# Optimization experiments

Measured on AMD Instinct MI355X. Metric: run time of the kernel, lower is better.

Reference implementation:

```python
import jax, jax.numpy as jnp
import numpy as np

NUM_GROUPS = 32
NUM_HEAD_CH = 64
EPS = 1e-5


def setup_inputs() -> dict:
    key = jax.random.key(0)
    k1, k2, k3 = jax.random.split(key, 3)
    B, C, H, W = 16, 512, 32, 32
    return {
        "x": jax.random.normal(k1, (B, C, H, W), dtype=jnp.float32),
        "norm_w": jnp.ones((C,), dtype=jnp.float32),
        "norm_b": jnp.zeros((C,), dtype=jnp.float32),
        "qkv_w": jax.random.normal(k2, (3 * C, C), dtype=jnp.float32) * 0.02,
        "qkv_b": jnp.zeros((3 * C,), dtype=jnp.float32),
        "proj_w": jax.random.normal(k3, (C, C), dtype=jnp.float32) * 0.02,
        "proj_b": jnp.zeros((C,), dtype=jnp.float32),
    }


def _group_norm(x, w, b):
    # x: [B, C, T]
    B, C, T = x.shape
    g = x.reshape(B, NUM_GROUPS, C // NUM_GROUPS, T)
    mean = g.mean(axis=(2, 3), keepdims=True)
    var = g.var(axis=(2, 3), keepdims=True)
    g = (g - mean) * jax.lax.rsqrt(var + EPS)
    return g.reshape(B, C, T) * w[None, :, None] + b[None, :, None]


def reference(x, norm_w, norm_b, qkv_w, qkv_b, proj_w, proj_b):
    B, C, Hs, Ws = x.shape
    T = Hs * Ws
    xr = x.reshape(B, C, T)
    xn = _group_norm(xr, norm_w, norm_b)
    # 1x1 conv == matmul over channel dim
    qkv = jnp.einsum('oc,bct->bot', qkv_w, xn) + qkv_b[None, :, None]  # [B, 3C, T]
    q, k, v = jnp.split(qkv, 3, axis=1)
    nH = C // NUM_HEAD_CH
    ch = NUM_HEAD_CH
    q = q.reshape(B * nH, ch, T)
    k = k.reshape(B * nH, ch, T)
    v = v.reshape(B * nH, ch, T)
    scale = 1.0 / np.sqrt(np.sqrt(ch)).astype(np.float32)
    # [BH, T, S] score matrix, softmax in float32 (matches torch .float())
    weight = jnp.einsum('bct,bcs->bts', q * scale, k * scale)
    weight = jax.nn.softmax(weight.astype(jnp.float32), axis=-1).astype(weight.dtype)
    a = jnp.einsum('bts,bcs->bct', weight, v).reshape(B, C, T)
    h = jnp.einsum('oc,bct->bot', proj_w, a) + proj_b[None, :, None]
    return (xr + h).reshape(B, C, Hs, Ws)
```

## Files before the change

kernel.cpp:

```cpp
#include <hip/hip_runtime.h>
#include <hip/hip_bf16.h>


typedef __bf16 bf16x8 __attribute__((ext_vector_type(8)));
typedef __bf16 bf16x4 __attribute__((ext_vector_type(4)));
typedef float f32x4 __attribute__((ext_vector_type(4)));

#define MFMA16(a, b, c) __builtin_amdgcn_mfma_f32_16x16x32_bf16((a), (b), (c), 0, 0, 0)

typedef const __attribute__((address_space(1))) unsigned int* gptr_t;
typedef __attribute__((address_space(3))) unsigned int* lptr_t;

__device__ __forceinline__ void gload16(const void* g, void* l) {
  __builtin_amdgcn_global_load_lds((gptr_t)g, (lptr_t)l, 16, 0, 0);
}

__global__ __launch_bounds__(256) void cvt_bf16_2(const float* __restrict__ s0,
                                                  __hip_bfloat16* __restrict__ d0,
                                                  int n0,
                                                  const float* __restrict__ s1,
                                                  __hip_bfloat16* __restrict__ d1,
                                                  int n1) {
  int i = blockIdx.x * 256 + threadIdx.x;
  const float* src;
  __hip_bfloat16* dst;
  if (i < n0) {
    src = s0; dst = d0;
  } else {
    i -= n0;
    if (i >= n1) return;
    src = s1; dst = d1;
  }
  float4 v = ((const float4*)src)[i];
  union { __hip_bfloat16 h[4]; uint2 u; } pk;
  pk.h[0] = __float2bfloat16(v.x);
  pk.h[1] = __float2bfloat16(v.y);
  pk.h[2] = __float2bfloat16(v.z);
  pk.h[3] = __float2bfloat16(v.w);
  *(uint2*)(dst + (size_t)i * 4) = pk.u;
}

__global__ __launch_bounds__(256) void gn_kernel(const float* __restrict__ x,
                                                 const float* __restrict__ nw,
                                                 const float* __restrict__ nb,
                                                 __hip_bfloat16* __restrict__ xnt) {
  const int blk = blockIdx.x;
  const int bb = blk >> 5, g = blk & 31;
  const int tid = threadIdx.x;
  const float4* xg = (const float4*)(x + ((size_t)bb * 512 + g * 16) * 1024);

  float4 vals[16];
  float s = 0.f, ss = 0.f;
#pragma unroll
  for (int k = 0; k < 16; ++k) {
    float4 v = xg[tid + 256 * k];
    vals[k] = v;
    s += v.x + v.y + v.z + v.w;
    ss += v.x * v.x + v.y * v.y + v.z * v.z + v.w * v.w;
  }
#pragma unroll
  for (int off = 1; off < 64; off <<= 1) {
    s += __shfl_xor(s, off, 64);
    ss += __shfl_xor(ss, off, 64);
  }
  __shared__ float red[8];
  const int wid = tid >> 6, lane = tid & 63;
  if (lane == 0) { red[wid] = s; red[wid + 4] = ss; }
  __syncthreads();
  s = red[0] + red[1] + red[2] + red[3];
  ss = red[4] + red[5] + red[6] + red[7];
  const float mean = s * (1.f / 16384.f);
  const float var = ss * (1.f / 16384.f) - mean * mean;
  const float rstd = rsqrtf(var + 1e-5f);

  float aa[16], cc[16];
#pragma unroll
  for (int k = 0; k < 16; ++k) {
    float w = nw[g * 16 + k];
    float b = nb[g * 16 + k];
    aa[k] = rstd * w;
    cc[k] = b - mean * aa[k];
  }
#pragma unroll
  for (int j = 0; j < 4; ++j) {
    union { __hip_bfloat16 h[16]; uint4 u[2]; } row;
#pragma unroll
    for (int k = 0; k < 16; ++k) {
      float v = ((const float*)&vals[k])[j];
      row.h[k] = __float2bfloat16(v * aa[k] + cc[k]);
    }
    size_t idx = ((size_t)bb * 1024 + 4 * tid + j) * 512 + g * 16;
    *(uint4*)(xnt + idx) = row.u[0];
    *(uint4*)(xnt + idx + 8) = row.u[1];
  }
}

template <int EPI>
__global__ __launch_bounds__(512) void gemm_bt(const __hip_bfloat16* __restrict__ A,
                                               const __hip_bfloat16* __restrict__ Bt,
                                               const float* __restrict__ bias,
                                               __hip_bfloat16* __restrict__ oq,
                                               __hip_bfloat16* __restrict__ ok,
                                               __hip_bfloat16* __restrict__ ov,
                                               const float* __restrict__ xres,
                                               float* __restrict__ of) {
  __shared__ __hip_bfloat16 Alds[128 * 64];
  __shared__ __hip_bfloat16 Blds[256 * 64];
  const int tid = threadIdx.x;
  const int wid = tid >> 6, lane = tid & 63;
  const int g = lane >> 4, tl = lane & 15;
  const int wr = wid >> 2, wc = wid & 3;
  const int NM = (EPI == 0) ? 12 : 4;
  const int id = blockIdx.x;
  const int xcd = id & 7, w = id >> 3;
  const int m0 = (w % NM) * 128;
  const int n0 = (xcd * 8 + w / NM) * 256;

  const int srow8 = lane >> 3;
  const int sselem = ((lane & 7) * 8) ^ (srow8 << 3);
  const int rswz = (tl & 7) << 4;

  f32x4 acc[4][4];
#pragma unroll
  for (int i = 0; i < 4; ++i)
#pragma unroll
    for (int j = 0; j < 4; ++j) acc[i][j] = (f32x4){0.f, 0.f, 0.f, 0.f};

  for (int kt = 0; kt < 8; ++kt) {
    const int k0 = kt * 64;
    __syncthreads();
#pragma unroll
    for (int q = 0; q < 2; ++q) {
      const int r = q * 64 + wid * 8 + srow8;
      gload16(A + (size_t)(m0 + r) * 512 + k0 + sselem,
              (char*)Alds + q * 8192 + wid * 1024);
    }
#pragma unroll
    for (int q = 0; q < 4; ++q) {
      const int r = q * 64 + wid * 8 + srow8;
      gload16(Bt + (size_t)(n0 + r) * 512 + k0 + sselem,
              (char*)Blds + q * 8192 + wid * 1024);
    }
    __syncthreads();
#pragma unroll
    for (int kk = 0; kk < 2; ++kk) {
      bf16x8 af[4], bfr[4];
#pragma unroll
      for (int mi = 0; mi < 4; ++mi) {
        const int row = wr * 64 + mi * 16 + tl;
        af[mi] = *(const bf16x8*)((char*)Alds + row * 128 + ((kk * 64 + g * 16) ^ rswz));
      }
#pragma unroll
      for (int ni = 0; ni < 4; ++ni) {
        const int row = wc * 64 + ni * 16 + tl;
        bfr[ni] = *(const bf16x8*)((char*)Blds + row * 128 + ((kk * 64 + g * 16) ^ rswz));
      }
      __builtin_amdgcn_s_setprio(1);
#pragma unroll
      for (int mi = 0; mi < 4; ++mi)
#pragma unroll
        for (int ni = 0; ni < 4; ++ni)
          acc[mi][ni] = MFMA16(af[mi], bfr[ni], acc[mi][ni]);
      __builtin_amdgcn_s_setprio(0);
    }
  }

  if (EPI == 0) {
    const bool isv = (m0 >= 1024);
    const bool isq = (m0 < 512);
    const float qs = 0.42466090014286f;
#pragma unroll
    for (int mi = 0; mi < 4; ++mi) {
      const int o = m0 + wr * 64 + mi * 16 + g * 4;
      const int och = o & 511, h = och >> 6, cb = och & 63;
#pragma unroll
      for (int ni = 0; ni < 4; ++ni) {
        const int n = n0 + wc * 64 + ni * 16 + tl;
        const int bb2 = n >> 10, t = n & 1023;
        const int bh = bb2 * 8 + h;
        if (!isv) {
          union { __hip_bfloat16 h4[4]; uint2 u; } pk;
#pragma unroll
          for (int r = 0; r < 4; ++r)
            pk.h4[r] = __float2bfloat16((acc[mi][ni][r] + bias[o + r]) * qs);
          __hip_bfloat16* dst = (isq ? oq : ok) + ((size_t)bh * 1024 + t) * 64 + cb;
          *(uint2*)dst = pk.u;
        } else {
#pragma unroll
          for (int r = 0; r < 4; ++r)
            ov[((size_t)bh * 64 + cb + r) * 1024 + t] =
                __float2bfloat16(acc[mi][ni][r] + bias[o + r]);
        }
      }
    }
  } else {
#pragma unroll
    for (int mi = 0; mi < 4; ++mi) {
#pragma unroll
      for (int r = 0; r < 4; ++r) {
        const int o = m0 + wr * 64 + mi * 16 + g * 4 + r;
        const float bv = bias[o];
#pragma unroll
        for (int ni = 0; ni < 4; ++ni) {
          const int n = n0 + wc * 64 + ni * 16 + tl;
          const int bb2 = n >> 10, t = n & 1023;
          const size_t xi = ((size_t)bb2 * 512 + o) * 1024 + t;
          of[xi] = xres[xi] + acc[mi][ni][r] + bv;
        }
      }
    }
  }
}

__global__ __launch_bounds__(512) void attn_kernel(const __hip_bfloat16* __restrict__ qt,
                                                   const __hip_bfloat16* __restrict__ kt,
                                                   const __hip_bfloat16* __restrict__ vv,
                                                   __hip_bfloat16* __restrict__ at) {
  const int blk = blockIdx.x;
  const int xcd = blk & 7;
  const int within = blk >> 3;
  const int tile = within & 3;
  const int bhi = xcd * 16 + (within >> 2);
  const int tid = threadIdx.x;
  const int wid = tid >> 6, lane = tid & 63;
  const int g = lane >> 4, tl = lane & 15;
  const int t0 = tile * 256 + wid * 32;

  const char* qh = (const char*)(qt + (size_t)bhi * 65536);
  const char* kh = (const char*)(kt + (size_t)bhi * 65536);
  const char* vh = (const char*)(vv + (size_t)bhi * 65536);

  __shared__ __hip_bfloat16 Klds[2][4096];
  __shared__ __hip_bfloat16 Vlds[2][4096];
  __shared__ __hip_bfloat16 Plds[8][2048];

  const int swz = (tl & 7) << 4;
  char* Pw = (char*)&Plds[wid][0];

  const int srow = lane >> 3;
  const int ssw = ((lane & 7) * 16) ^ (srow << 4);
  const int rb0 = wid * 8;

  bf16x8 qb[2][2];
#pragma unroll
  for (int qs = 0; qs < 2; ++qs)
#pragma unroll
    for (int h = 0; h < 2; ++h)
      qb[qs][h] = *(const bf16x8*)(qh + (size_t)(t0 + qs * 16 + tl) * 128 + h * 64 + g * 16);

  bf16x8 vones;
#pragma unroll
  for (int i = 0; i < 8; ++i) vones[i] = (__bf16)1.0f;

  f32x4 acc[2][4];
  f32x4 accl[2];
#pragma unroll
  for (int i = 0; i < 2; ++i) {
    accl[i] = (f32x4){0.f, 0.f, 0.f, 0.f};
#pragma unroll
    for (int j = 0; j < 4; ++j) acc[i][j] = (f32x4){0.f, 0.f, 0.f, 0.f};
  }

  {
    const int r = rb0 + srow;
    gload16(kh + (size_t)r * 128 + ssw, (char*)&Klds[0][0] + rb0 * 128);
    gload16(vh + (size_t)r * 2048 + ssw, (char*)&Vlds[0][0] + rb0 * 128);
  }
  __syncthreads();

  int cur = 0;
  for (int sb = 0; sb < 16; ++sb) {
    if (sb < 15) {
      const int s0n = (sb + 1) * 64;
      const int r = rb0 + srow;
      gload16(kh + (size_t)(s0n + r) * 128 + ssw, (char*)&Klds[cur ^ 1][0] + rb0 * 128);
      gload16(vh + (size_t)r * 2048 + s0n * 2 + ssw, (char*)&Vlds[cur ^ 1][0] + rb0 * 128);
    }
    const char* Kb = (const char*)&Klds[cur][0];
    const char* Vb = (const char*)&Vlds[cur][0];

    f32x4 sv[4][2];
#pragma unroll
    for (int st = 0; st < 4; ++st) {
      const int krow = (st * 16 + tl) * 128;
      bf16x8 ka0 = *(const bf16x8*)(Kb + krow + ((g * 16) ^ swz));
      bf16x8 ka1 = *(const bf16x8*)(Kb + krow + ((64 + g * 16) ^ swz));
      __builtin_amdgcn_s_setprio(1);
#pragma unroll
      for (int qs = 0; qs < 2; ++qs) {
        f32x4 z = (f32x4){0.f, 0.f, 0.f, 0.f};
        z = MFMA16(ka0, qb[qs][0], z);
        z = MFMA16(ka1, qb[qs][1], z);
        sv[st][qs] = z;
      }
      __builtin_amdgcn_s_setprio(0);
    }

#pragma unroll
    for (int qs = 0; qs < 2; ++qs) {
#pragma unroll
      for (int st = 0; st < 4; ++st) {
        bf16x4 pu;
#pragma unroll
        for (int r = 0; r < 4; ++r) {
          float p = exp2f(sv[st][qs][r]);
          pu[r] = (__bf16)p;
        }
        *(bf16x4*)(Pw + (qs * 16 + tl) * 128 + ((st * 32 + g * 8) ^ swz)) = pu;
      }
    }

    bf16x8 pa[2][2];
#pragma unroll
    for (int ts = 0; ts < 2; ++ts) {
      const int prow = (ts * 16 + tl) * 128;
      pa[ts][0] = *(const bf16x8*)(Pw + prow + ((g * 16) ^ swz));
      pa[ts][1] = *(const bf16x8*)(Pw + prow + ((64 + g * 16) ^ swz));
    }
    __builtin_amdgcn_s_setprio(1);
#pragma unroll
    for (int ts = 0; ts < 2; ++ts) {
      accl[ts] = MFMA16(pa[ts][0], vones, accl[ts]);
      accl[ts] = MFMA16(pa[ts][1], vones, accl[ts]);
    }
    __builtin_amdgcn_s_setprio(0);
#pragma unroll
    for (int ct = 0; ct < 4; ++ct) {
      const int vrow = (ct * 16 + tl) * 128;
      bf16x8 vb0 = *(const bf16x8*)(Vb + vrow + ((g * 16) ^ swz));
      bf16x8 vb1 = *(const bf16x8*)(Vb + vrow + ((64 + g * 16) ^ swz));
      __builtin_amdgcn_s_setprio(1);
#pragma unroll
      for (int ts = 0; ts < 2; ++ts) {
        acc[ts][ct] = MFMA16(pa[ts][0], vb0, acc[ts][ct]);
        acc[ts][ct] = MFMA16(pa[ts][1], vb1, acc[ts][ct]);
      }
      __builtin_amdgcn_s_setprio(0);
    }
    __syncthreads();
    cur ^= 1;
  }

  const int bb2 = bhi >> 3, hh = bhi & 7;
#pragma unroll
  for (int ts = 0; ts < 2; ++ts) {
#pragma unroll
    for (int r = 0; r < 4; ++r) {
      const float iv = 1.f / accl[ts][r];
      const size_t row = (size_t)bb2 * 1024 + t0 + ts * 16 + g * 4 + r;
#pragma unroll
      for (int ct = 0; ct < 4; ++ct)
        at[row * 512 + hh * 64 + ct * 16 + tl] = __float2bfloat16(acc[ts][ct][r] * iv);
    }
  }
}

extern "C" void kernel_launch(void* const* d_in, const int* in_sizes, int n_in,
                              void* d_out, int out_size, void* d_ws, size_t ws_size,
                              hipStream_t stream) {
  const float* x  = (const float*)d_in[0];
  const float* nw = (const float*)d_in[1];
  const float* nb = (const float*)d_in[2];
  const float* qw = (const float*)d_in[3];
  const float* qb = (const float*)d_in[4];
  const float* pw = (const float*)d_in[5];
  const float* pb = (const float*)d_in[6];
  float* out = (float*)d_out;
  char* ws = (char*)d_ws;

  __hip_bfloat16* xnt = (__hip_bfloat16*)(ws);
  __hip_bfloat16* qtb = (__hip_bfloat16*)(ws + 16777216);
  __hip_bfloat16* ktb = (__hip_bfloat16*)(ws + 33554432);
  __hip_bfloat16* vvb = (__hip_bfloat16*)(ws + 50331648);
  __hip_bfloat16* qwb = (__hip_bfloat16*)(ws + 67108864);
  __hip_bfloat16* pwb = (__hip_bfloat16*)(ws + 68681728);

  cvt_bf16_2<<<1024, 256, 0, stream>>>(qw, qwb, 196608, pw, pwb, 65536);
  gn_kernel<<<512, 256, 0, stream>>>(x, nw, nb, xnt);
  gemm_bt<0><<<768, 512, 0, stream>>>(qwb, xnt, qb, qtb, ktb, vvb,
                                      nullptr, nullptr);
  attn_kernel<<<512, 512, 0, stream>>>(qtb, ktb, vvb, xnt);
  gemm_bt<1><<<256, 512, 0, stream>>>(pwb, xnt, pb, nullptr, nullptr,
                                      nullptr, x, out);
}
```

Before: 141.3 us.

## Halve attention tile per block, drop LDS double buffering, double grid

The attention kernel now gives each wave 16 query rows instead of 32. It launches 1024 blocks instead of 512, with single-buffered K/V tiles in LDS and a smaller P scratch, and a min-blocks launch bound. This cuts registers and LDS per block so more blocks fit per CU and more waves hide latency. The cost is losing the software prefetch overlap, adding an extra barrier per step, and reloading each K/V tile for half as many queries, which doubles K/V traffic. The group-norm block index mapping is also swapped so consecutive blocks cover different batches.

```diff
diff --git a/kernel.cpp b/kernel.cpp
--- a/kernel.cpp
+++ b/kernel.cpp
@@ -45,7 +45,7 @@
                                                  const float* __restrict__ nb,
                                                  __hip_bfloat16* __restrict__ xnt) {
   const int blk = blockIdx.x;
-  const int bb = blk >> 5, g = blk & 31;
+  const int bb = blk & 15, g = blk >> 4;
   const int tid = threadIdx.x;
   const float4* xg = (const float4*)(x + ((size_t)bb * 512 + g * 16) * 1024);
 
@@ -212,146 +212,103 @@
   }
 }
 
-__global__ __launch_bounds__(512) void attn_kernel(const __hip_bfloat16* __restrict__ qt,
-                                                   const __hip_bfloat16* __restrict__ kt,
-                                                   const __hip_bfloat16* __restrict__ vv,
-                                                   __hip_bfloat16* __restrict__ at) {
+__global__ __launch_bounds__(512, 8) void attn_kernel(
+    const __hip_bfloat16* __restrict__ qt,
+    const __hip_bfloat16* __restrict__ kt,
+    const __hip_bfloat16* __restrict__ vv,
+    __hip_bfloat16* __restrict__ at) {
   const int blk = blockIdx.x;
   const int xcd = blk & 7;
   const int within = blk >> 3;
-  const int tile = within & 3;
-  const int bhi = xcd * 16 + (within >> 2);
+  const int tile = within & 7;
+  const int bhi = xcd * 16 + (within >> 3);
   const int tid = threadIdx.x;
   const int wid = tid >> 6, lane = tid & 63;
   const int g = lane >> 4, tl = lane & 15;
-  const int t0 = tile * 256 + wid * 32;
+  const int t0 = tile * 128 + wid * 16;
 
   const char* qh = (const char*)(qt + (size_t)bhi * 65536);
   const char* kh = (const char*)(kt + (size_t)bhi * 65536);
   const char* vh = (const char*)(vv + (size_t)bhi * 65536);
 
-  __shared__ __hip_bfloat16 Klds[2][4096];
-  __shared__ __hip_bfloat16 Vlds[2][4096];
-  __shared__ __hip_bfloat16 Plds[8][2048];
+  __shared__ __hip_bfloat16 Klds[4096];
+  __shared__ __hip_bfloat16 Vlds[4096];
+  __shared__ __hip_bfloat16 Plds[8][1024];
 
   const int swz = (tl & 7) << 4;
   char* Pw = (char*)&Plds[wid][0];
 
   const int srow = lane >> 3;
-  const int ssw = ((lane & 7) * 16) ^ (srow << 4);
-  const int rb0 = wid * 8;
-
-  bf16x8 qb[2][2];
-#pragma unroll
-  for (int qs = 0; qs < 2; ++qs)
-#pragma unroll
-    for (int h = 0; h < 2; ++h)
-      qb[qs][h] = *(const bf16x8*)(qh + (size_t)(t0 + qs * 16 + tl) * 128 + h * 64 + g * 16);
+  const int grow = wid * 8 + srow;
+  const int ssw = ((lane & 7) * 16) ^ ((srow & 7) << 4);
+
+  bf16x8 qb0 = *(const bf16x8*)(qh + (size_t)(t0 + tl) * 128 + g * 16);
+  bf16x8 qb1 = *(const bf16x8*)(qh + (size_t)(t0 + tl) * 128 + 64 + g * 16);
 
   bf16x8 vones;
 #pragma unroll
   for (int i = 0; i < 8; ++i) vones[i] = (__bf16)1.0f;
 
-  f32x4 acc[2][4];
-  f32x4 accl[2];
-#pragma unroll
-  for (int i = 0; i < 2; ++i) {
-    accl[i] = (f32x4){0.f, 0.f, 0.f, 0.f};
-#pragma unroll
-    for (int j = 0; j < 4; ++j) acc[i][j] = (f32x4){0.f, 0.f, 0.f, 0.f};
-  }
-
-  {
-    const int r = rb0 + srow;
-    gload16(kh + (size_t)r * 128 + ssw, (char*)&Klds[0][0] + rb0 * 128);
-    gload16(vh + (size_t)r * 2048 + ssw, (char*)&Vlds[0][0] + rb0 * 128);
-  }
-  __syncthreads();
-
-  int cur = 0;
+  f32x4 acc[4];
+  f32x4 accl = (f32x4){0.f, 0.f, 0.f, 0.f};
+#pragma unroll
+  for (int j = 0; j < 4; ++j) acc[j] = (f32x4){0.f, 0.f, 0.f, 0.f};
+
   for (int sb = 0; sb < 16; ++sb) {
-    if (sb < 15) {
-      const int s0n = (sb + 1) * 64;
-      const int r = rb0 + srow;
-      gload16(kh + (size_t)(s0n + r) * 128 + ssw, (char*)&Klds[cur ^ 1][0] + rb0 * 128);
-      gload16(vh + (size_t)r * 2048 + s0n * 2 + ssw, (char*)&Vlds[cur ^ 1][0] + rb0 * 128);
-    }
-    const char* Kb = (const char*)&Klds[cur][0];
-    const char* Vb = (const char*)&Vlds[cur][0];
-
-    f32x4 sv[4][2];
+    const int s0 = sb * 64;
+    __syncthreads();
+    gload16(kh + (size_t)(s0 + grow) * 128 + ssw, (char*)Klds + wid * 1024);
+    gload16(vh + (size_t)grow * 2048 + s0 * 2 + ssw, (char*)Vlds + wid * 1024);
+    __syncthreads();
+
+    f32x4 sv[4];
 #pragma unroll
     for (int st = 0; st < 4; ++st) {
       const int krow = (st * 16 + tl) * 128;
-      bf16x8 ka0 = *(const bf16x8*)(Kb + krow + ((g * 16) ^ swz));
-      bf16x8 ka1 = *(const bf16x8*)(Kb + krow + ((64 + g * 16) ^ swz));
+      bf16x8 ka0 = *(const bf16x8*)((char*)Klds + krow + ((g * 16) ^ swz));
+      bf16x8 ka1 = *(const bf16x8*)((char*)Klds + krow + ((64 + g * 16) ^ swz));
       __builtin_amdgcn_s_setprio(1);
-#pragma unroll
-      for (int qs = 0; qs < 2; ++qs) {
-        f32x4 z = (f32x4){0.f, 0.f, 0.f, 0.f};
-        z = MFMA16(ka0, qb[qs][0], z);
-        z = MFMA16(ka1, qb[qs][1], z);
-        sv[st][qs] = z;
-      }
+      f32x4 z = (f32x4){0.f, 0.f, 0.f, 0.f};
+      z = MFMA16(ka0, qb0, z);
+      z = MFMA16(ka1, qb1, z);
       __builtin_amdgcn_s_setprio(0);
-    }
-
-#pragma unroll
-    for (int qs = 0; qs < 2; ++qs) {
-#pragma unroll
-      for (int st = 0; st < 4; ++st) {
-        bf16x4 pu;
-#pragma unroll
-        for (int r = 0; r < 4; ++r) {
-          float p = exp2f(sv[st][qs][r]);
-          pu[r] = (__bf16)p;
-        }
-        *(bf16x4*)(Pw + (qs * 16 + tl) * 128 + ((st * 32 + g * 8) ^ swz)) = pu;
-      }
-    }
-
-    bf16x8 pa[2][2];
-#pragma unroll
-    for (int ts = 0; ts < 2; ++ts) {
-      const int prow = (ts * 16 + tl) * 128;
-      pa[ts][0] = *(const bf16x8*)(Pw + prow + ((g * 16) ^ swz));
-      pa[ts][1] = *(const bf16x8*)(Pw + prow + ((64 + g * 16) ^ swz));
-    }
+      sv[st] = z;
+    }
+
+#pragma unroll
+    for (int st = 0; st < 4; ++st) {
+      bf16x4 pu;
+#pragma unroll
+      for (int r = 0; r < 4; ++r) pu[r] = (__bf16)exp2f(sv[st][r]);
+      *(bf16x4*)(Pw + tl * 128 + ((st * 32 + g * 8) ^ swz)) = pu;
+    }
+    bf16x8 pa0 = *(const bf16x8*)(Pw + tl * 128 + ((g * 16) ^ swz));
+    bf16x8 pa1 = *(const bf16x8*)(Pw + tl * 128 + ((64 + g * 16) ^ swz));
+
     __builtin_amdgcn_s_setprio(1);
-#pragma unroll
-    for (int ts = 0; ts < 2; ++ts) {
-      accl[ts] = MFMA16(pa[ts][0], vones, accl[ts]);
-      accl[ts] = MFMA16(pa[ts][1], vones, accl[ts]);
-    }
+    accl = MFMA16(pa0, vones, accl);
+    accl = MFMA16(pa1, vones, accl);
     __builtin_amdgcn_s_setprio(0);
 #pragma unroll
     for (int ct = 0; ct < 4; ++ct) {
       const int vrow = (ct * 16 + tl) * 128;
-      bf16x8 vb0 = *(const bf16x8*)(Vb + vrow + ((g * 16) ^ swz));
-      bf16x8 vb1 = *(const bf16x8*)(Vb + vrow + ((64 + g * 16) ^ swz));
+      bf16x8 vb0 = *(const bf16x8*)((char*)Vlds + vrow + ((g * 16) ^ swz));
+      bf16x8 vb1 = *(const bf16x8*)((char*)Vlds + vrow + ((64 + g * 16) ^ swz));
       __builtin_amdgcn_s_setprio(1);
-#pragma unroll
-      for (int ts = 0; ts < 2; ++ts) {
-        acc[ts][ct] = MFMA16(pa[ts][0], vb0, acc[ts][ct]);
-        acc[ts][ct] = MFMA16(pa[ts][1], vb1, acc[ts][ct]);
-      }
+      acc[ct] = MFMA16(pa0, vb0, acc[ct]);
+      acc[ct] = MFMA16(pa1, vb1, acc[ct]);
       __builtin_amdgcn_s_setprio(0);
     }
-    __syncthreads();
-    cur ^= 1;
   }
 
   const int bb2 = bhi >> 3, hh = bhi & 7;
 #pragma unroll
-  for (int ts = 0; ts < 2; ++ts) {
-#pragma unroll
-    for (int r = 0; r < 4; ++r) {
-      const float iv = 1.f / accl[ts][r];
-      const size_t row = (size_t)bb2 * 1024 + t0 + ts * 16 + g * 4 + r;
-#pragma unroll
-      for (int ct = 0; ct < 4; ++ct)
-        at[row * 512 + hh * 64 + ct * 16 + tl] = __float2bfloat16(acc[ts][ct][r] * iv);
-    }
+  for (int r = 0; r < 4; ++r) {
+    const float iv = 1.f / accl[r];
+    const size_t row = (size_t)bb2 * 1024 + t0 + g * 4 + r;
+#pragma unroll
+    for (int ct = 0; ct < 4; ++ct)
+      at[row * 512 + hh * 64 + ct * 16 + tl] = __float2bfloat16(acc[ct][r] * iv);
   }
 }
 
@@ -379,7 +336,7 @@
   gn_kernel<<<512, 256, 0, stream>>>(x, nw, nb, xnt);
   gemm_bt<0><<<768, 512, 0, stream>>>(qwb, xnt, qb, qtb, ktb, vvb,
                                       nullptr, nullptr);
-  attn_kernel<<<512, 512, 0, stream>>>(qtb, ktb, vvb, xnt);
+  attn_kernel<<<1024, 512, 0, stream>>>(qtb, ktb, vvb, xnt);
   gemm_bt<1><<<256, 512, 0, stream>>>(pwb, xnt, pb, nullptr, nullptr,
                                       nullptr, x, out);
 }
```

After: 147.1 us. 4.1% more time.

## Fuse weight conversion into groupnorm launch and triple-buffer attention K/V loads

Applied to the files above, without the earlier changes.

Merges the bf16 weight-conversion kernel into the group-norm kernel as extra blocks, removing one launch, and remaps group-norm block indexing to batch-minor order. In the attention kernel, K/V tiles move from double to triple buffering with a prefetch distance of two, and full __syncthreads are replaced by a partial vmcnt wait plus a barrier. The aim is to hide global-to-LDS load latency behind the MFMA work, at the cost of more LDS per block, which may lower occupancy. The loop also issues wrapped-around loads past the last tile, which are redundant.

```diff
diff --git a/kernel.cpp b/kernel.cpp
--- a/kernel.cpp
+++ b/kernel.cpp
@@ -15,37 +15,35 @@
   __builtin_amdgcn_global_load_lds((gptr_t)g, (lptr_t)l, 16, 0, 0);
 }
 
-__global__ __launch_bounds__(256) void cvt_bf16_2(const float* __restrict__ s0,
-                                                  __hip_bfloat16* __restrict__ d0,
-                                                  int n0,
-                                                  const float* __restrict__ s1,
-                                                  __hip_bfloat16* __restrict__ d1,
-                                                  int n1) {
-  int i = blockIdx.x * 256 + threadIdx.x;
-  const float* src;
-  __hip_bfloat16* dst;
-  if (i < n0) {
-    src = s0; dst = d0;
-  } else {
-    i -= n0;
-    if (i >= n1) return;
-    src = s1; dst = d1;
-  }
-  float4 v = ((const float4*)src)[i];
-  union { __hip_bfloat16 h[4]; uint2 u; } pk;
-  pk.h[0] = __float2bfloat16(v.x);
-  pk.h[1] = __float2bfloat16(v.y);
-  pk.h[2] = __float2bfloat16(v.z);
-  pk.h[3] = __float2bfloat16(v.w);
-  *(uint2*)(dst + (size_t)i * 4) = pk.u;
-}
-
-__global__ __launch_bounds__(256) void gn_kernel(const float* __restrict__ x,
-                                                 const float* __restrict__ nw,
-                                                 const float* __restrict__ nb,
-                                                 __hip_bfloat16* __restrict__ xnt) {
+__global__ __launch_bounds__(256) void gn_cvt_kernel(const float* __restrict__ x,
+                                                     const float* __restrict__ nw,
+                                                     const float* __restrict__ nb,
+                                                     __hip_bfloat16* __restrict__ xnt,
+                                                     const float* __restrict__ qw,
+                                                     __hip_bfloat16* __restrict__ qwb,
+                                                     const float* __restrict__ pw,
+                                                     __hip_bfloat16* __restrict__ pwb) {
   const int blk = blockIdx.x;
-  const int bb = blk >> 5, g = blk & 31;
+  if (blk >= 512) {
+    const int base = (blk - 512) * 256 + threadIdx.x;
+#pragma unroll
+    for (int t = 0; t < 4; ++t) {
+      int i = base + t * 65536;
+      const float* src;
+      __hip_bfloat16* dst;
+      if (i < 196608) { src = qw; dst = qwb; }
+      else            { i -= 196608; src = pw; dst = pwb; }
+      float4 v = ((const float4*)src)[i];
+      union { __hip_bfloat16 h[4]; uint2 u; } pk;
+      pk.h[0] = __float2bfloat16(v.x);
+      pk.h[1] = __float2bfloat16(v.y);
+      pk.h[2] = __float2bfloat16(v.z);
+      pk.h[3] = __float2bfloat16(v.w);
+      *(uint2*)(dst + (size_t)i * 4) = pk.u;
+    }
+    return;
+  }
+  const int bb = blk & 15, g = blk >> 4;
   const int tid = threadIdx.x;
   const float4* xg = (const float4*)(x + ((size_t)bb * 512 + g * 16) * 1024);
 
@@ -212,10 +210,11 @@
   }
 }
 
-__global__ __launch_bounds__(512) void attn_kernel(const __hip_bfloat16* __restrict__ qt,
-                                                   const __hip_bfloat16* __restrict__ kt,
-                                                   const __hip_bfloat16* __restrict__ vv,
-                                                   __hip_bfloat16* __restrict__ at) {
+__global__ __launch_bounds__(512) void attn_kernel(
+    const __hip_bfloat16* __restrict__ qt,
+    const __hip_bfloat16* __restrict__ kt,
+    const __hip_bfloat16* __restrict__ vv,
+    __hip_bfloat16* __restrict__ at) {
   const int blk = blockIdx.x;
   const int xcd = blk & 7;
   const int within = blk >> 3;
@@ -230,16 +229,16 @@
   const char* kh = (const char*)(kt + (size_t)bhi * 65536);
   const char* vh = (const char*)(vv + (size_t)bhi * 65536);
 
-  __shared__ __hip_bfloat16 Klds[2][4096];
-  __shared__ __hip_bfloat16 Vlds[2][4096];
+  __shared__ __hip_bfloat16 Klds[3][4096];
+  __shared__ __hip_bfloat16 Vlds[3][4096];
   __shared__ __hip_bfloat16 Plds[8][2048];
 
   const int swz = (tl & 7) << 4;
   char* Pw = (char*)&Plds[wid][0];
 
   const int srow = lane >> 3;
-  const int ssw = ((lane & 7) * 16) ^ (srow << 4);
-  const int rb0 = wid * 8;
+  const int grow = wid * 8 + srow;
+  const int ssw = ((lane & 7) * 16) ^ ((srow & 7) << 4);
 
   bf16x8 qb[2][2];
 #pragma unroll
@@ -261,23 +260,25 @@
     for (int j = 0; j < 4; ++j) acc[i][j] = (f32x4){0.f, 0.f, 0.f, 0.f};
   }
 
-  {
-    const int r = rb0 + srow;
-    gload16(kh + (size_t)r * 128 + ssw, (char*)&Klds[0][0] + rb0 * 128);
-    gload16(vh + (size_t)r * 2048 + ssw, (char*)&Vlds[0][0] + rb0 * 128);
-  }
-  __syncthreads();
-
-  int cur = 0;
+  gload16(kh + (size_t)grow * 128 + ssw, (char*)&Klds[0][0] + wid * 1024);
+  gload16(vh + (size_t)grow * 2048 + ssw, (char*)&Vlds[0][0] + wid * 1024);
+  gload16(kh + (size_t)(64 + grow) * 128 + ssw, (char*)&Klds[1][0] + wid * 1024);
+  gload16(vh + (size_t)grow * 2048 + 128 + ssw, (char*)&Vlds[1][0] + wid * 1024);
+  asm volatile("s_waitcnt vmcnt(2)" ::: "memory");
+  __builtin_amdgcn_s_barrier();
+
   for (int sb = 0; sb < 16; ++sb) {
-    if (sb < 15) {
-      const int s0n = (sb + 1) * 64;
-      const int r = rb0 + srow;
-      gload16(kh + (size_t)(s0n + r) * 128 + ssw, (char*)&Klds[cur ^ 1][0] + rb0 * 128);
-      gload16(vh + (size_t)r * 2048 + s0n * 2 + ssw, (char*)&Vlds[cur ^ 1][0] + rb0 * 128);
-    }
-    const char* Kb = (const char*)&Klds[cur][0];
-    const char* Vb = (const char*)&Vlds[cur][0];
+    {
+      const int nt = (sb + 2) & 15;
+      const int nbuf = (sb + 2) % 3;
+      gload16(kh + (size_t)(nt * 64 + grow) * 128 + ssw,
+              (char*)&Klds[nbuf][0] + wid * 1024);
+      gload16(vh + (size_t)grow * 2048 + nt * 128 + ssw,
+              (char*)&Vlds[nbuf][0] + wid * 1024);
+    }
+    const int cb = sb % 3;
+    const char* Kb = (const char*)&Klds[cb][0];
+    const char* Vb = (const char*)&Vlds[cb][0];
 
     f32x4 sv[4][2];
 #pragma unroll
@@ -337,8 +338,8 @@
       }
       __builtin_amdgcn_s_setprio(0);
     }
-    __syncthreads();
-    cur ^= 1;
+    asm volatile("s_waitcnt vmcnt(2)" ::: "memory");
+    __builtin_amdgcn_s_barrier();
   }
 
   const int bb2 = bhi >> 3, hh = bhi & 7;
@@ -375,8 +376,7 @@
   __hip_bfloat16* qwb = (__hip_bfloat16*)(ws + 67108864);
   __hip_bfloat16* pwb = (__hip_bfloat16*)(ws + 68681728);
 
-  cvt_bf16_2<<<1024, 256, 0, stream>>>(qw, qwb, 196608, pw, pwb, 65536);
-  gn_kernel<<<512, 256, 0, stream>>>(x, nw, nb, xnt);
+  gn_cvt_kernel<<<768, 256, 0, stream>>>(x, nw, nb, xnt, qw, qwb, pw, pwb);
   gemm_bt<0><<<768, 512, 0, stream>>>(qwb, xnt, qb, qtb, ktb, vvb,
                                       nullptr, nullptr);
   attn_kernel<<<512, 512, 0, stream>>>(qtb, ktb, vvb, xnt);
```

Result: faster. 136.3 us (-3.6%).
